# Performance work log

Hardware: AMD Instinct MI355X
Metric: run time of the kernel (lower is better)

The kernel has to match this reference:

```python
import jax, jax.numpy as jnp
import numpy as np
from jax.scipy.special import logsumexp

NEG = -10000.0  # LARGENUMBER in the torch code (finite, avoids NaN grads)


def _inside_Z(rules, sequence_lengths):
    """Log-semiring CKY inside algorithm (the `coolio` path of the torch module).

    rules: (B, S, S) span mention scores.
    chart[b,i,j] = inside score of span [i, j] where each span multiplies in
    (1 + exp(rule)) i.e. adds softplus(rule) (mention OR non-mention), and
    binarization sums over split points:
        chart[i,i] = softplus(rules[i,i])
        chart[i,j] = softplus(rules[i,j]) + logsumexp_{k=i..j-1}(chart[i,k] + chart[k+1,j])
    This matches: initial inside_s = logsumexp([rules, 0]) on the upper triangle,
    then width-wise logbmminside + diagonal add of log1p(exp(rules)).
    """
    B, S, _ = rules.shape
    idx = jnp.arange(S)
    sp = jax.nn.softplus(rules)  # log1p(exp(rules)), stable
    chart0 = jnp.full((B, S, S), NEG, dtype=rules.dtype)
    chart0 = chart0.at[:, idx, idx].set(jnp.diagonal(sp, axis1=1, axis2=2))

    def step(chart, w):
        # end position j = i + w (clipped; clipped rows are masked out below)
        j = jnp.clip(idx + w, 0, S - 1)                      # (S,)
        right = jnp.take(chart, j, axis=2)                   # right[b,k,i] = chart[b,k,i+w]
        right = jnp.concatenate([right[:, 1:, :], jnp.full_like(right[:, :1, :], NEG)], axis=1)  # chart[b,k+1,i+w]
        # scores[b,i,k] = chart[b,i,k] + chart[b,k+1,i+w]
        scores = chart + jnp.swapaxes(right, 1, 2)
        # valid split points: i <= k < i + w
        kmask = (idx[None, :] >= idx[:, None]) & (idx[None, :] < idx[:, None] + w)
        scores = jnp.where(kmask[None], scores, NEG)
        new_diag = logsumexp(scores, axis=2) + sp[:, idx, j]  # (B, S)
        valid = (idx + w) < S
        old = chart[:, idx, j]
        chart = chart.at[:, idx, j].set(jnp.where(valid[None, :], new_diag, old))
        return chart, None

    chart, _ = jax.lax.scan(step, chart0, jnp.arange(1, S))
    Z = chart[jnp.arange(B), 0, sequence_lengths - 1]  # log partition per sentence
    return Z


def setup_inputs():
    key = jax.random.key(0)
    k1, k2 = jax.random.split(key)
    B, S = 16, 192
    span = jax.random.normal(k1, (B, S, S, 1), dtype=jnp.float32)
    lens = jax.random.randint(k2, (B,), S // 2, S + 1).astype(jnp.int32)
    lens = lens.at[0].set(S)  # max length equals padded dim, as the torch module assumes
    return {"span_mention_score_matrix": span, "sequence_lengths": lens}


def reference(span_mention_score_matrix, sequence_lengths):
    # score_dim == 1 -> squeeze; marginal = d(sum Z)/d(rules), as in torch.autograd.grad
    rules = span_mention_score_matrix[..., 0]

    def f(r):
        Z = _inside_Z(r, sequence_lengths)
        return Z.sum(), Z

    (_, Z), marginal = jax.value_and_grad(f, has_aux=True)(rules)
    return Z, marginal
```

## Files before the change

kernel.cpp:

```cpp
#include <hip/hip_runtime.h>


#define SS 192
#define BB 16
#define TT 16
#define NTL 12
#define NEGF (-1e30f)

__device__ __forceinline__ float softplusf(float x) {
  return fmaxf(x, 0.f) + log1pf(__expf(-fabsf(x)));
}
__device__ __forceinline__ void lse_merge(float& m, float& s, float m2, float s2) {
  float nm = fmaxf(m, m2);
  s = s * __expf(m - nm) + s2 * __expf(m2 - nm);
  m = nm;
}
template <int CTRL>
__device__ __forceinline__ float dppf(float x) {
  return __int_as_float(__builtin_amdgcn_update_dpp(
      0, __float_as_int(x), CTRL, 0xF, 0xF, true));
}

__global__ __launch_bounds__(256) void init_od(float* __restrict__ odG,
                                               float* __restrict__ odTG) {
  const int n4 = BB * SS * SS / 4;
  float4 nf = make_float4(NEGF, NEGF, NEGF, NEGF);
  float4* a = reinterpret_cast<float4*>(odG);
  float4* c = reinterpret_cast<float4*>(odTG);
  for (int i = blockIdx.x * 256 + threadIdx.x; i < n4; i += gridDim.x * 256) {
    a[i] = nf; c[i] = nf;
  }
}

__global__ __launch_bounds__(256) void inside_diag(const float* __restrict__ rules,
                                                   float* __restrict__ chG_,
                                                   float* __restrict__ chTG_,
                                                   int d) {
  const int ntiles = NTL - d;
  const int b = blockIdx.x / ntiles;
  const int I = blockIdx.x % ntiles;
  const int J = I + d;
  const int tid = threadIdx.x;
  const int ci = tid >> 4, cj = tid & 15;
  const int gi = TT * I + ci, gj = TT * J + cj;
  const float* __restrict__ R = rules + (size_t)b * SS * SS;
  float* __restrict__ chG  = chG_  + (size_t)b * SS * SS;
  float* __restrict__ chTG = chTG_ + (size_t)b * SS * SS;

  __shared__ float A[TT][TT + 1], Bt[TT][TT + 1], T[TT][TT + 1];
  __shared__ float P[TT][TT + 1], SP[TT][TT + 1];
  __shared__ float brow[TT];

  const float spv_own = softplusf(R[gi * SS + gj]);
  SP[ci][cj] = spv_own;
  T[ci][cj] = (d == 0 && ci == cj) ? spv_own : NEGF;
  if (d >= 1) {
    A[ci][cj]  = chG[(TT * I + ci) * SS + TT * I + cj];
    Bt[ci][cj] = chG[(TT * J + ci) * SS + TT * J + cj];
  }
  if (d >= 2 && tid < TT) brow[tid] = chG[(TT * (I + 1)) * SS + TT * J + tid];

  {
    float m = NEGF, s = 0.f;
    const float* chRow  = chG  + gi * SS;
    const float* chTRow = chTG + gj * SS;
    const int k0 = TT * (I + 1), k1 = TT * J;
    if (k0 < k1) {
      float4 blo = *reinterpret_cast<const float4*>(chTRow + k0);
      for (int k = k0; k < k1; k += 4) {
        float4 a4  = *reinterpret_cast<const float4*>(chRow + k);
        float4 bhi = *reinterpret_cast<const float4*>(chTRow + k + 4);
        float v0 = a4.x + blo.y, v1 = a4.y + blo.z;
        float v2 = a4.z + blo.w, v3 = a4.w + bhi.x;
        float bm = fmaxf(fmaxf(v0, v1), fmaxf(v2, v3));
        float bs = __expf(v0 - bm) + __expf(v1 - bm) +
                   __expf(v2 - bm) + __expf(v3 - bm);
        lse_merge(m, s, bm, bs);
        blo = bhi;
      }
    }
    P[ci][cj] = (m < -1e29f) ? NEGF : m + __logf(s);
  }
  __syncthreads();

  if (tid < 64) {
    const int cidx = tid >> 2, g = tid & 3;
    const int s0 = (d == 0) ? TT : 0;
    for (int st = s0; st <= 30; ++st) {
      int ilmin = 15 - st; if (ilmin < 0) ilmin = 0;
      int ilmax = 30 - st; if (ilmax > 15) ilmax = 15;
      bool act = (cidx <= ilmax - ilmin);
      int tci = ilmin + (act ? cidx : 0);
      int tcj = tci + st - 15;
      int c1 = (d == 0) ? (st - 15) : (TT - tci);
      int c2 = (d == 0) ? 0 : tcj;
      int nt = c1 + c2;
      float m  = (g == 0) ? P[tci][tcj] : NEGF;
      float sa = (g == 0) ? 1.f : 0.f;
      float tv[8];
      #pragma unroll
      for (int u = 0; u < 8; ++u) {
        int t = g + 4 * u;
        bool ok = act && (t < nt);
        int tc = ok ? t : 0;
        float va, vb;
        if (tc < c1) {
          int kk = tci + tc;
          va = (d == 0) ? T[tci][kk] : A[tci][kk];
          int r2 = kk + 1;
          if (r2 <= 15) vb = T[r2][tcj];
          else          vb = (d == 1) ? Bt[0][tcj] : brow[tcj];
        } else {
          int tp = tc - c1;
          va = T[tci][tp];
          vb = Bt[tp + 1][tcj];
        }
        tv[u] = ok ? (va + vb) : NEGF;
      }
      float m0 = fmaxf(tv[0], tv[1]), m1 = fmaxf(tv[2], tv[3]);
      float m2 = fmaxf(tv[4], tv[5]), m3 = fmaxf(tv[6], tv[7]);
      float bm = fmaxf(fmaxf(m0, m1), fmaxf(m2, m3));
      float bs = (__expf(tv[0] - bm) + __expf(tv[1] - bm)) +
                 (__expf(tv[2] - bm) + __expf(tv[3] - bm)) +
                 (__expf(tv[4] - bm) + __expf(tv[5] - bm)) +
                 (__expf(tv[6] - bm) + __expf(tv[7] - bm));
      lse_merge(m, sa, bm, bs);
      lse_merge(m, sa, dppf<0xB1>(m), dppf<0xB1>(sa));
      lse_merge(m, sa, dppf<0x4E>(m), dppf<0x4E>(sa));
      if (act && g == 0)
        T[tci][tcj] = SP[tci][tcj] + m + __logf(sa);
      __builtin_amdgcn_wave_barrier();
    }
  }
  __syncthreads();
  chG [gi * SS + gj] = T[ci][cj];
  chTG[gj * SS + gi] = T[ci][cj];
}

__global__ __launch_bounds__(256) void outside_diag(const float* __restrict__ rules,
                                                    const int* __restrict__ lens,
                                                    const float* __restrict__ chG_,
                                                    const float* __restrict__ chTG_,
                                                    float* __restrict__ odG_,
                                                    float* __restrict__ odTG_,
                                                    int d) {
  const int ntiles = NTL - d;
  const int b = blockIdx.x / ntiles;
  const int I = blockIdx.x % ntiles;
  const int J = I + d;
  const int L = lens[b];
  if (TT * J >= L) return;
  const int tid = threadIdx.x;
  const int ci = tid >> 4, cj = tid & 15;
  const int gi = TT * I + ci, gj = TT * J + cj;
  const float* __restrict__ R = rules + (size_t)b * SS * SS;
  const float* __restrict__ chG  = chG_  + (size_t)b * SS * SS;
  const float* __restrict__ chTG = chTG_ + (size_t)b * SS * SS;
  float* __restrict__ odG  = odG_  + (size_t)b * SS * SS;
  float* __restrict__ odTG = odTG_ + (size_t)b * SS * SS;

  __shared__ float A[TT][TT + 1], Bt[TT][TT + 1], T[TT][TT + 1];
  __shared__ float P[TT][TT + 1], SP[TT][TT + 1];

  const float spv_own = softplusf(R[gi * SS + gj]);
  SP[ci][cj] = spv_own;
  A[ci][cj]  = chG[(TT * I + ci) * SS + TT * I + cj];
  Bt[ci][cj] = chG[(TT * J + ci) * SS + TT * J + cj];
  const bool isroot = (gi == 0) && (gj == L - 1);
  T[ci][cj] = isroot ? spv_own : NEGF;

  {
    float m = NEGF, s = 0.f;
    const float* odRow    = odG + gi * SS;
    const float* chRowJ1  = chG + (gj + 1) * SS;
    const int p0 = TT * (J + 1);
    for (int p = p0; p < SS; p += 4) {
      float4 o4 = *reinterpret_cast<const float4*>(odRow + p);
      float4 c4 = *reinterpret_cast<const float4*>(chRowJ1 + p);
      float v0 = o4.x + c4.x, v1 = o4.y + c4.y;
      float v2 = o4.z + c4.z, v3 = o4.w + c4.w;
      float bm = fmaxf(fmaxf(v0, v1), fmaxf(v2, v3));
      float bs = __expf(v0 - bm) + __expf(v1 - bm) +
                 __expf(v2 - bm) + __expf(v3 - bm);
      lse_merge(m, s, bm, bs);
    }
    const float* odTRow   = odTG + gj * SS;
    const float* chTRowI1 = chTG + (gi - 1) * SS;
    const int aEnd = TT * I;
    for (int a = 0; a < aEnd; a += 4) {
      float4 o4 = *reinterpret_cast<const float4*>(odTRow + a);
      float4 c4 = *reinterpret_cast<const float4*>(chTRowI1 + a);
      float v0 = o4.x + c4.x, v1 = o4.y + c4.y;
      float v2 = o4.z + c4.z, v3 = o4.w + c4.w;
      float bm = fmaxf(fmaxf(v0, v1), fmaxf(v2, v3));
      float bs = __expf(v0 - bm) + __expf(v1 - bm) +
                 __expf(v2 - bm) + __expf(v3 - bm);
      lse_merge(m, s, bm, bs);
    }
    P[ci][cj] = (m < -1e29f) ? NEGF : m + __logf(s);
  }
  __syncthreads();

  if (tid < 64) {
    const int cidx = tid >> 2, g = tid & 3;
    const int sEnd = (d == 0) ? 15 : 0;
    for (int st = 30; st >= sEnd; --st) {
      int ilmin = 15 - st; if (ilmin < 0) ilmin = 0;
      int ilmax = 30 - st; if (ilmax > 15) ilmax = 15;
      bool act = (cidx <= ilmax - ilmin);
      int tci = ilmin + (act ? cidx : 0);
      int tcj = tci + st - 15;
      int tgi = TT * I + tci, tgj = TT * J + tcj;
      bool rooted = (tgi == 0 && tgj == L - 1);
      bool dowrite = act && (tgj < L) && !rooted;
      int c1 = 15 - tcj, c2 = tci;
      int nt = c1 + c2;
      float m  = (g == 0) ? P[tci][tcj] : NEGF;
      float sa = (g == 0) ? 1.f : 0.f;
      int cim1 = (tci > 0) ? tci - 1 : 0;
      float tv[8];
      #pragma unroll
      for (int u = 0; u < 8; ++u) {
        int t = g + 4 * u;
        bool ok = act && (t < nt);
        int tc = ok ? t : 0;
        float va, vb;
        if (tc < c1) {
          int pl = tcj + 1 + tc;
          va = T[tci][pl];
          vb = Bt[tcj + 1][pl];
        } else {
          int al = tc - c1;
          va = T[al][tcj];
          vb = A[al][cim1];
        }
        tv[u] = ok ? (va + vb) : NEGF;
      }
      float m0 = fmaxf(tv[0], tv[1]), m1 = fmaxf(tv[2], tv[3]);
      float m2 = fmaxf(tv[4], tv[5]), m3 = fmaxf(tv[6], tv[7]);
      float bm = fmaxf(fmaxf(m0, m1), fmaxf(m2, m3));
      float bs = (__expf(tv[0] - bm) + __expf(tv[1] - bm)) +
                 (__expf(tv[2] - bm) + __expf(tv[3] - bm)) +
                 (__expf(tv[4] - bm) + __expf(tv[5] - bm)) +
                 (__expf(tv[6] - bm) + __expf(tv[7] - bm));
      lse_merge(m, sa, bm, bs);
      lse_merge(m, sa, dppf<0xB1>(m), dppf<0xB1>(sa));
      lse_merge(m, sa, dppf<0x4E>(m), dppf<0x4E>(sa));
      if (dowrite && g == 0)
        T[tci][tcj] = SP[tci][tcj] + m + __logf(sa);
      __builtin_amdgcn_wave_barrier();
    }
  }
  __syncthreads();
  odG [gi * SS + gj] = T[ci][cj];
  odTG[gj * SS + gi] = T[ci][cj];
}

__global__ __launch_bounds__(256) void cky_marg(const float* __restrict__ rules,
                                                const int* __restrict__ lens,
                                                const float* __restrict__ chG_,
                                                const float* __restrict__ odG_,
                                                float* __restrict__ outZ,
                                                float* __restrict__ marg) {
  const int total = BB * SS * SS;
  for (int idx = blockIdx.x * 256 + threadIdx.x; idx < total; idx += gridDim.x * 256) {
    int b = idx / (SS * SS);
    int rem = idx - b * SS * SS;
    int i = rem / SS, j = rem - i * SS;
    int L = lens[b];
    if (rem == 0) outZ[b] = chG_[(size_t)b * SS * SS + (L - 1)];
    float val = 0.f;
    if (i <= j && j < L) {
      float r = rules[idx];
      float sp = softplusf(r);
      float Z = chG_[(size_t)b * SS * SS + (L - 1)];
      float o = odG_[idx] - sp;
      float c = chG_[idx];
      float sig = 1.f / (1.f + __expf(-r));
      val = sig * __expf(o + c - Z);
    }
    marg[idx] = val;
  }
}

extern "C" void kernel_launch(void* const* d_in, const int* in_sizes, int n_in,
                              void* d_out, int out_size, void* d_ws, size_t ws_size,
                              hipStream_t stream) {
  const float* rules = (const float*)d_in[0];
  const int* lens = (const int*)d_in[1];
  float* outZ = (float*)d_out;
  float* marg = (float*)d_out + BB;

  float* chG_  = (float*)d_ws;
  float* chTG_ = chG_  + (size_t)BB * SS * SS;
  float* odG_  = chTG_ + (size_t)BB * SS * SS;
  float* odTG_ = odG_  + (size_t)BB * SS * SS;

  init_od<<<256, 256, 0, stream>>>(odG_, odTG_);
  for (int d = 0; d < NTL; ++d)
    inside_diag<<<BB * (NTL - d), 256, 0, stream>>>(rules, chG_, chTG_, d);
  for (int d = NTL - 1; d >= 0; --d)
    outside_diag<<<BB * (NTL - d), 256, 0, stream>>>(rules, lens, chG_, chTG_,
                                                     odG_, odTG_, d);
  cky_marg<<<(BB * SS * SS + 255) / 256, 256, 0, stream>>>(rules, lens, chG_,
                                                           odG_, outZ, marg);
}
```

Measured before the change: 931.5 us.

## Fuse all CKY diagonal launches into one cooperative kernel with grid syncs

Replaces the 26 separate kernel launches (init, 12 inside diagonals, 12 outside diagonals, marginal) with a single cooperative kernel of BB*NTL blocks that loops over diagonals and uses grid-wide syncs between them. This is meant to remove per-launch overhead and inter-kernel gaps, which dominate for these small, latency-bound diagonal steps. In exchange, the final marginal pass and the init now run on only 192 blocks, and grid.sync carries its own cost.

```diff
diff --git a/kernel.cpp b/kernel.cpp
--- a/kernel.cpp
+++ b/kernel.cpp
@@ -1,10 +1,14 @@
 #include <hip/hip_runtime.h>
-
+#include <hip/hip_cooperative_groups.h>
+
+
+namespace cg = cooperative_groups;
 
 #define SS 192
 #define BB 16
 #define TT 16
 #define NTL 12
+#define NBLK (BB * NTL)
 #define NEGF (-1e30f)
 
 __device__ __forceinline__ float softplusf(float x) {
@@ -21,265 +25,263 @@
       0, __float_as_int(x), CTRL, 0xF, 0xF, true));
 }
 
-__global__ __launch_bounds__(256) void init_od(float* __restrict__ odG,
-                                               float* __restrict__ odTG) {
-  const int n4 = BB * SS * SS / 4;
-  float4 nf = make_float4(NEGF, NEGF, NEGF, NEGF);
-  float4* a = reinterpret_cast<float4*>(odG);
-  float4* c = reinterpret_cast<float4*>(odTG);
-  for (int i = blockIdx.x * 256 + threadIdx.x; i < n4; i += gridDim.x * 256) {
-    a[i] = nf; c[i] = nf;
-  }
-}
-
-__global__ __launch_bounds__(256) void inside_diag(const float* __restrict__ rules,
-                                                   float* __restrict__ chG_,
-                                                   float* __restrict__ chTG_,
-                                                   int d) {
-  const int ntiles = NTL - d;
-  const int b = blockIdx.x / ntiles;
-  const int I = blockIdx.x % ntiles;
-  const int J = I + d;
+__global__ __launch_bounds__(256) void cky_all(const float* __restrict__ rules,
+                                               const int* __restrict__ lens,
+                                               float* __restrict__ chGb,
+                                               float* __restrict__ chTGb,
+                                               float* __restrict__ odGb,
+                                               float* __restrict__ odTGb,
+                                               float* __restrict__ outZ,
+                                               float* __restrict__ marg) {
+  cg::grid_group grid = cg::this_grid();
+  const int bid = blockIdx.x;
   const int tid = threadIdx.x;
   const int ci = tid >> 4, cj = tid & 15;
-  const int gi = TT * I + ci, gj = TT * J + cj;
-  const float* __restrict__ R = rules + (size_t)b * SS * SS;
-  float* __restrict__ chG  = chG_  + (size_t)b * SS * SS;
-  float* __restrict__ chTG = chTG_ + (size_t)b * SS * SS;
 
   __shared__ float A[TT][TT + 1], Bt[TT][TT + 1], T[TT][TT + 1];
   __shared__ float P[TT][TT + 1], SP[TT][TT + 1];
   __shared__ float brow[TT];
 
-  const float spv_own = softplusf(R[gi * SS + gj]);
-  SP[ci][cj] = spv_own;
-  T[ci][cj] = (d == 0 && ci == cj) ? spv_own : NEGF;
-  if (d >= 1) {
-    A[ci][cj]  = chG[(TT * I + ci) * SS + TT * I + cj];
-    Bt[ci][cj] = chG[(TT * J + ci) * SS + TT * J + cj];
+  {
+    const int n4 = BB * SS * SS / 4;
+    float4 nf = make_float4(NEGF, NEGF, NEGF, NEGF);
+    float4* a = reinterpret_cast<float4*>(odGb);
+    float4* c = reinterpret_cast<float4*>(odTGb);
+    for (int i = bid * 256 + tid; i < n4; i += NBLK * 256) { a[i] = nf; c[i] = nf; }
   }
-  if (d >= 2 && tid < TT) brow[tid] = chG[(TT * (I + 1)) * SS + TT * J + tid];
+  grid.sync();
+
+  for (int d = 0; d < NTL; ++d) {
+    const int ntiles = NTL - d;
+    if (bid < BB * ntiles) {
+      const int b = bid / ntiles;
+      const int I = bid % ntiles;
+      const int J = I + d;
+      const int gi = TT * I + ci, gj = TT * J + cj;
+      const float* __restrict__ R = rules + (size_t)b * SS * SS;
+      float* __restrict__ chG  = chGb  + (size_t)b * SS * SS;
+      float* __restrict__ chTG = chTGb + (size_t)b * SS * SS;
+
+      const float spv_own = softplusf(R[gi * SS + gj]);
+      SP[ci][cj] = spv_own;
+      T[ci][cj] = (d == 0 && ci == cj) ? spv_own : NEGF;
+      if (d >= 1) {
+        A[ci][cj]  = chG[(TT * I + ci) * SS + TT * I + cj];
+        Bt[ci][cj] = chG[(TT * J + ci) * SS + TT * J + cj];
+      }
+      if (d >= 2 && tid < TT) brow[tid] = chG[(TT * (I + 1)) * SS + TT * J + tid];
+
+      {
+        float m = NEGF, s = 0.f;
+        const float* chRow  = chG  + gi * SS;
+        const float* chTRow = chTG + gj * SS;
+        const int k0 = TT * (I + 1), k1 = TT * J;
+        if (k0 < k1) {
+          float4 blo = *reinterpret_cast<const float4*>(chTRow + k0);
+          for (int k = k0; k < k1; k += 4) {
+            float4 a4  = *reinterpret_cast<const float4*>(chRow + k);
+            float4 bhi = *reinterpret_cast<const float4*>(chTRow + k + 4);
+            float v0 = a4.x + blo.y, v1 = a4.y + blo.z;
+            float v2 = a4.z + blo.w, v3 = a4.w + bhi.x;
+            float bm = fmaxf(fmaxf(v0, v1), fmaxf(v2, v3));
+            float bs = __expf(v0 - bm) + __expf(v1 - bm) +
+                       __expf(v2 - bm) + __expf(v3 - bm);
+            lse_merge(m, s, bm, bs);
+            blo = bhi;
+          }
+        }
+        P[ci][cj] = (m < -1e29f) ? NEGF : m + __logf(s);
+      }
+      __syncthreads();
+
+      if (tid < 64) {
+        const int cidx = tid >> 2, g = tid & 3;
+        const int s0 = (d == 0) ? TT : 0;
+        for (int st = s0; st <= 30; ++st) {
+          int ilmin = 15 - st; if (ilmin < 0) ilmin = 0;
+          int ilmax = 30 - st; if (ilmax > 15) ilmax = 15;
+          bool act = (cidx <= ilmax - ilmin);
+          int tci = ilmin + (act ? cidx : 0);
+          int tcj = tci + st - 15;
+          int c1 = (d == 0) ? (st - 15) : (TT - tci);
+          int c2 = (d == 0) ? 0 : tcj;
+          int nt = c1 + c2;
+          float m  = (g == 0) ? P[tci][tcj] : NEGF;
+          float sa = (g == 0) ? 1.f : 0.f;
+          float tv[8];
+          #pragma unroll
+          for (int u = 0; u < 8; ++u) {
+            int t = g + 4 * u;
+            bool ok = act && (t < nt);
+            int tc = ok ? t : 0;
+            float va, vb;
+            if (tc < c1) {
+              int kk = tci + tc;
+              va = (d == 0) ? T[tci][kk] : A[tci][kk];
+              int r2 = kk + 1;
+              if (r2 <= 15) vb = T[r2][tcj];
+              else          vb = (d == 1) ? Bt[0][tcj] : brow[tcj];
+            } else {
+              int tp = tc - c1;
+              va = T[tci][tp];
+              vb = Bt[tp + 1][tcj];
+            }
+            tv[u] = ok ? (va + vb) : NEGF;
+          }
+          float m0 = fmaxf(tv[0], tv[1]), m1 = fmaxf(tv[2], tv[3]);
+          float m2 = fmaxf(tv[4], tv[5]), m3 = fmaxf(tv[6], tv[7]);
+          float bm = fmaxf(fmaxf(m0, m1), fmaxf(m2, m3));
+          float bs = (__expf(tv[0] - bm) + __expf(tv[1] - bm)) +
+                     (__expf(tv[2] - bm) + __expf(tv[3] - bm)) +
+                     (__expf(tv[4] - bm) + __expf(tv[5] - bm)) +
+                     (__expf(tv[6] - bm) + __expf(tv[7] - bm));
+          lse_merge(m, sa, bm, bs);
+          lse_merge(m, sa, dppf<0xB1>(m), dppf<0xB1>(sa));
+          lse_merge(m, sa, dppf<0x4E>(m), dppf<0x4E>(sa));
+          if (act && g == 0)
+            T[tci][tcj] = SP[tci][tcj] + m + __logf(sa);
+          __builtin_amdgcn_wave_barrier();
+        }
+      }
+      __syncthreads();
+      chG [gi * SS + gj] = T[ci][cj];
+      chTG[gj * SS + gi] = T[ci][cj];
+    }
+    grid.sync();
+  }
+
+  for (int d = NTL - 1; d >= 0; --d) {
+    const int ntiles = NTL - d;
+    if (bid < BB * ntiles) {
+      const int b = bid / ntiles;
+      const int I = bid % ntiles;
+      const int J = I + d;
+      const int L = lens[b];
+      if (TT * J < L) {
+        const int gi = TT * I + ci, gj = TT * J + cj;
+        const float* __restrict__ R = rules + (size_t)b * SS * SS;
+        const float* __restrict__ chG  = chGb  + (size_t)b * SS * SS;
+        const float* __restrict__ chTG = chTGb + (size_t)b * SS * SS;
+        float* __restrict__ odG  = odGb  + (size_t)b * SS * SS;
+        float* __restrict__ odTG = odTGb + (size_t)b * SS * SS;
+
+        const float spv_own = softplusf(R[gi * SS + gj]);
+        SP[ci][cj] = spv_own;
+        A[ci][cj]  = chG[(TT * I + ci) * SS + TT * I + cj];
+        Bt[ci][cj] = chG[(TT * J + ci) * SS + TT * J + cj];
+        const bool isroot = (gi == 0) && (gj == L - 1);
+        T[ci][cj] = isroot ? spv_own : NEGF;
+
+        {
+          float m = NEGF, s = 0.f;
+          const float* odRow   = odG + gi * SS;
+          const float* chRowJ1 = chG + (gj + 1) * SS;
+          const int p0 = TT * (J + 1);
+          for (int p = p0; p < SS; p += 4) {
+            float4 o4 = *reinterpret_cast<const float4*>(odRow + p);
+            float4 c4 = *reinterpret_cast<const float4*>(chRowJ1 + p);
+            float v0 = o4.x + c4.x, v1 = o4.y + c4.y;
+            float v2 = o4.z + c4.z, v3 = o4.w + c4.w;
+            float bm = fmaxf(fmaxf(v0, v1), fmaxf(v2, v3));
+            float bs = __expf(v0 - bm) + __expf(v1 - bm) +
+                       __expf(v2 - bm) + __expf(v3 - bm);
+            lse_merge(m, s, bm, bs);
+          }
+          const float* odTRow   = odTG + gj * SS;
+          const float* chTRowI1 = chTG + (gi - 1) * SS;
+          const int aEnd = TT * I;
+          for (int a = 0; a < aEnd; a += 4) {
+            float4 o4 = *reinterpret_cast<const float4*>(odTRow + a);
+            float4 c4 = *reinterpret_cast<const float4*>(chTRowI1 + a);
+            float v0 = o4.x + c4.x, v1 = o4.y + c4.y;
+            float v2 = o4.z + c4.z, v3 = o4.w + c4.w;
+            float bm = fmaxf(fmaxf(v0, v1), fmaxf(v2, v3));
+            float bs = __expf(v0 - bm) + __expf(v1 - bm) +
+                       __expf(v2 - bm) + __expf(v3 - bm);
+            lse_merge(m, s, bm, bs);
+          }
+          P[ci][cj] = (m < -1e29f) ? NEGF : m + __logf(s);
+        }
+        __syncthreads();
+
+        if (tid < 64) {
+          const int cidx = tid >> 2, g = tid & 3;
+          const int sEnd = (d == 0) ? 15 : 0;
+          for (int st = 30; st >= sEnd; --st) {
+            int ilmin = 15 - st; if (ilmin < 0) ilmin = 0;
+            int ilmax = 30 - st; if (ilmax > 15) ilmax = 15;
+            bool act = (cidx <= ilmax - ilmin);
+            int tci = ilmin + (act ? cidx : 0);
+            int tcj = tci + st - 15;
+            int tgi = TT * I + tci, tgj = TT * J + tcj;
+            bool rooted = (tgi == 0 && tgj == L - 1);
+            bool dowrite = act && (tgj < L) && !rooted;
+            int c1 = 15 - tcj, c2 = tci;
+            int nt = c1 + c2;
+            float m  = (g == 0) ? P[tci][tcj] : NEGF;
+            float sa = (g == 0) ? 1.f : 0.f;
+            int cim1 = (tci > 0) ? tci - 1 : 0;
+            float tv[8];
+            #pragma unroll
+            for (int u = 0; u < 8; ++u) {
+              int t = g + 4 * u;
+              bool ok = act && (t < nt);
+              int tc = ok ? t : 0;
+              float va, vb;
+              if (tc < c1) {
+                int pl = tcj + 1 + tc;
+                va = T[tci][pl];
+                vb = Bt[tcj + 1][pl];
+              } else {
+                int al = tc - c1;
+                va = T[al][tcj];
+                vb = A[al][cim1];
+              }
+              tv[u] = ok ? (va + vb) : NEGF;
+            }
+            float m0 = fmaxf(tv[0], tv[1]), m1 = fmaxf(tv[2], tv[3]);
+            float m2 = fmaxf(tv[4], tv[5]), m3 = fmaxf(tv[6], tv[7]);
+            float bm = fmaxf(fmaxf(m0, m1), fmaxf(m2, m3));
+            float bs = (__expf(tv[0] - bm) + __expf(tv[1] - bm)) +
+                       (__expf(tv[2] - bm) + __expf(tv[3] - bm)) +
+                       (__expf(tv[4] - bm) + __expf(tv[5] - bm)) +
+                       (__expf(tv[6] - bm) + __expf(tv[7] - bm));
+            lse_merge(m, sa, bm, bs);
+            lse_merge(m, sa, dppf<0xB1>(m), dppf<0xB1>(sa));
+            lse_merge(m, sa, dppf<0x4E>(m), dppf<0x4E>(sa));
+            if (dowrite && g == 0)
+              T[tci][tcj] = SP[tci][tcj] + m + __logf(sa);
+            __builtin_amdgcn_wave_barrier();
+          }
+        }
+        __syncthreads();
+        odG [gi * SS + gj] = T[ci][cj];
+        odTG[gj * SS + gi] = T[ci][cj];
+      }
+    }
+    grid.sync();
+  }
 
   {
-    float m = NEGF, s = 0.f;
-    const float* chRow  = chG  + gi * SS;
-    const float* chTRow = chTG + gj * SS;
-    const int k0 = TT * (I + 1), k1 = TT * J;
-    if (k0 < k1) {
-      float4 blo = *reinterpret_cast<const float4*>(chTRow + k0);
-      for (int k = k0; k < k1; k += 4) {
-        float4 a4  = *reinterpret_cast<const float4*>(chRow + k);
-        float4 bhi = *reinterpret_cast<const float4*>(chTRow + k + 4);
-        float v0 = a4.x + blo.y, v1 = a4.y + blo.z;
-        float v2 = a4.z + blo.w, v3 = a4.w + bhi.x;
-        float bm = fmaxf(fmaxf(v0, v1), fmaxf(v2, v3));
-        float bs = __expf(v0 - bm) + __expf(v1 - bm) +
-                   __expf(v2 - bm) + __expf(v3 - bm);
-        lse_merge(m, s, bm, bs);
-        blo = bhi;
-      }
+    const int total = BB * SS * SS;
+    for (int idx = bid * 256 + tid; idx < total; idx += NBLK * 256) {
+      int b = idx / (SS * SS);
+      int rem = idx - b * SS * SS;
+      int i = rem / SS, j = rem - i * SS;
+      int L = lens[b];
+      if (rem == 0) outZ[b] = chGb[(size_t)b * SS * SS + (L - 1)];
+      float val = 0.f;
+      if (i <= j && j < L) {
+        float r = rules[idx];
+        float sp = softplusf(r);
+        float Z = chGb[(size_t)b * SS * SS + (L - 1)];
+        float o = odGb[idx] - sp;
+        float c = chGb[idx];
+        float sig = 1.f / (1.f + __expf(-r));
+        val = sig * __expf(o + c - Z);
+      }
+      marg[idx] = val;
     }
-    P[ci][cj] = (m < -1e29f) ? NEGF : m + __logf(s);
-  }
-  __syncthreads();
-
-  if (tid < 64) {
-    const int cidx = tid >> 2, g = tid & 3;
-    const int s0 = (d == 0) ? TT : 0;
-    for (int st = s0; st <= 30; ++st) {
-      int ilmin = 15 - st; if (ilmin < 0) ilmin = 0;
-      int ilmax = 30 - st; if (ilmax > 15) ilmax = 15;
-      bool act = (cidx <= ilmax - ilmin);
-      int tci = ilmin + (act ? cidx : 0);
-      int tcj = tci + st - 15;
-      int c1 = (d == 0) ? (st - 15) : (TT - tci);
-      int c2 = (d == 0) ? 0 : tcj;
-      int nt = c1 + c2;
-      float m  = (g == 0) ? P[tci][tcj] : NEGF;
-      float sa = (g == 0) ? 1.f : 0.f;
-      float tv[8];
-      #pragma unroll
-      for (int u = 0; u < 8; ++u) {
-        int t = g + 4 * u;
-        bool ok = act && (t < nt);
-        int tc = ok ? t : 0;
-        float va, vb;
-        if (tc < c1) {
-          int kk = tci + tc;
-          va = (d == 0) ? T[tci][kk] : A[tci][kk];
-          int r2 = kk + 1;
-          if (r2 <= 15) vb = T[r2][tcj];
-          else          vb = (d == 1) ? Bt[0][tcj] : brow[tcj];
-        } else {
-          int tp = tc - c1;
-          va = T[tci][tp];
-          vb = Bt[tp + 1][tcj];
-        }
-        tv[u] = ok ? (va + vb) : NEGF;
-      }
-      float m0 = fmaxf(tv[0], tv[1]), m1 = fmaxf(tv[2], tv[3]);
-      float m2 = fmaxf(tv[4], tv[5]), m3 = fmaxf(tv[6], tv[7]);
-      float bm = fmaxf(fmaxf(m0, m1), fmaxf(m2, m3));
-      float bs = (__expf(tv[0] - bm) + __expf(tv[1] - bm)) +
-                 (__expf(tv[2] - bm) + __expf(tv[3] - bm)) +
-                 (__expf(tv[4] - bm) + __expf(tv[5] - bm)) +
-                 (__expf(tv[6] - bm) + __expf(tv[7] - bm));
-      lse_merge(m, sa, bm, bs);
-      lse_merge(m, sa, dppf<0xB1>(m), dppf<0xB1>(sa));
-      lse_merge(m, sa, dppf<0x4E>(m), dppf<0x4E>(sa));
-      if (act && g == 0)
-        T[tci][tcj] = SP[tci][tcj] + m + __logf(sa);
-      __builtin_amdgcn_wave_barrier();
-    }
-  }
-  __syncthreads();
-  chG [gi * SS + gj] = T[ci][cj];
-  chTG[gj * SS + gi] = T[ci][cj];
-}
-
-__global__ __launch_bounds__(256) void outside_diag(const float* __restrict__ rules,
-                                                    const int* __restrict__ lens,
-                                                    const float* __restrict__ chG_,
-                                                    const float* __restrict__ chTG_,
-                                                    float* __restrict__ odG_,
-                                                    float* __restrict__ odTG_,
-                                                    int d) {
-  const int ntiles = NTL - d;
-  const int b = blockIdx.x / ntiles;
-  const int I = blockIdx.x % ntiles;
-  const int J = I + d;
-  const int L = lens[b];
-  if (TT * J >= L) return;
-  const int tid = threadIdx.x;
-  const int ci = tid >> 4, cj = tid & 15;
-  const int gi = TT * I + ci, gj = TT * J + cj;
-  const float* __restrict__ R = rules + (size_t)b * SS * SS;
-  const float* __restrict__ chG  = chG_  + (size_t)b * SS * SS;
-  const float* __restrict__ chTG = chTG_ + (size_t)b * SS * SS;
-  float* __restrict__ odG  = odG_  + (size_t)b * SS * SS;
-  float* __restrict__ odTG = odTG_ + (size_t)b * SS * SS;
-
-  __shared__ float A[TT][TT + 1], Bt[TT][TT + 1], T[TT][TT + 1];
-  __shared__ float P[TT][TT + 1], SP[TT][TT + 1];
-
-  const float spv_own = softplusf(R[gi * SS + gj]);
-  SP[ci][cj] = spv_own;
-  A[ci][cj]  = chG[(TT * I + ci) * SS + TT * I + cj];
-  Bt[ci][cj] = chG[(TT * J + ci) * SS + TT * J + cj];
-  const bool isroot = (gi == 0) && (gj == L - 1);
-  T[ci][cj] = isroot ? spv_own : NEGF;
-
-  {
-    float m = NEGF, s = 0.f;
-    const float* odRow    = odG + gi * SS;
-    const float* chRowJ1  = chG + (gj + 1) * SS;
-    const int p0 = TT * (J + 1);
-    for (int p = p0; p < SS; p += 4) {
-      float4 o4 = *reinterpret_cast<const float4*>(odRow + p);
-      float4 c4 = *reinterpret_cast<const float4*>(chRowJ1 + p);
-      float v0 = o4.x + c4.x, v1 = o4.y + c4.y;
-      float v2 = o4.z + c4.z, v3 = o4.w + c4.w;
-      float bm = fmaxf(fmaxf(v0, v1), fmaxf(v2, v3));
-      float bs = __expf(v0 - bm) + __expf(v1 - bm) +
-                 __expf(v2 - bm) + __expf(v3 - bm);
-      lse_merge(m, s, bm, bs);
-    }
-    const float* odTRow   = odTG + gj * SS;
-    const float* chTRowI1 = chTG + (gi - 1) * SS;
-    const int aEnd = TT * I;
-    for (int a = 0; a < aEnd; a += 4) {
-      float4 o4 = *reinterpret_cast<const float4*>(odTRow + a);
-      float4 c4 = *reinterpret_cast<const float4*>(chTRowI1 + a);
-      float v0 = o4.x + c4.x, v1 = o4.y + c4.y;
-      float v2 = o4.z + c4.z, v3 = o4.w + c4.w;
-      float bm = fmaxf(fmaxf(v0, v1), fmaxf(v2, v3));
-      float bs = __expf(v0 - bm) + __expf(v1 - bm) +
-                 __expf(v2 - bm) + __expf(v3 - bm);
-      lse_merge(m, s, bm, bs);
-    }
-    P[ci][cj] = (m < -1e29f) ? NEGF : m + __logf(s);
-  }
-  __syncthreads();
-
-  if (tid < 64) {
-    const int cidx = tid >> 2, g = tid & 3;
-    const int sEnd = (d == 0) ? 15 : 0;
-    for (int st = 30; st >= sEnd; --st) {
-      int ilmin = 15 - st; if (ilmin < 0) ilmin = 0;
-      int ilmax = 30 - st; if (ilmax > 15) ilmax = 15;
-      bool act = (cidx <= ilmax - ilmin);
-      int tci = ilmin + (act ? cidx : 0);
-      int tcj = tci + st - 15;
-      int tgi = TT * I + tci, tgj = TT * J + tcj;
-      bool rooted = (tgi == 0 && tgj == L - 1);
-      bool dowrite = act && (tgj < L) && !rooted;
-      int c1 = 15 - tcj, c2 = tci;
-      int nt = c1 + c2;
-      float m  = (g == 0) ? P[tci][tcj] : NEGF;
-      float sa = (g == 0) ? 1.f : 0.f;
-      int cim1 = (tci > 0) ? tci - 1 : 0;
-      float tv[8];
-      #pragma unroll
-      for (int u = 0; u < 8; ++u) {
-        int t = g + 4 * u;
-        bool ok = act && (t < nt);
-        int tc = ok ? t : 0;
-        float va, vb;
-        if (tc < c1) {
-          int pl = tcj + 1 + tc;
-          va = T[tci][pl];
-          vb = Bt[tcj + 1][pl];
-        } else {
-          int al = tc - c1;
-          va = T[al][tcj];
-          vb = A[al][cim1];
-        }
-        tv[u] = ok ? (va + vb) : NEGF;
-      }
-      float m0 = fmaxf(tv[0], tv[1]), m1 = fmaxf(tv[2], tv[3]);
-      float m2 = fmaxf(tv[4], tv[5]), m3 = fmaxf(tv[6], tv[7]);
-      float bm = fmaxf(fmaxf(m0, m1), fmaxf(m2, m3));
-      float bs = (__expf(tv[0] - bm) + __expf(tv[1] - bm)) +
-                 (__expf(tv[2] - bm) + __expf(tv[3] - bm)) +
-                 (__expf(tv[4] - bm) + __expf(tv[5] - bm)) +
-                 (__expf(tv[6] - bm) + __expf(tv[7] - bm));
-      lse_merge(m, sa, bm, bs);
-      lse_merge(m, sa, dppf<0xB1>(m), dppf<0xB1>(sa));
-      lse_merge(m, sa, dppf<0x4E>(m), dppf<0x4E>(sa));
-      if (dowrite && g == 0)
-        T[tci][tcj] = SP[tci][tcj] + m + __logf(sa);
-      __builtin_amdgcn_wave_barrier();
-    }
-  }
-  __syncthreads();
-  odG [gi * SS + gj] = T[ci][cj];
-  odTG[gj * SS + gi] = T[ci][cj];
-}
-
-__global__ __launch_bounds__(256) void cky_marg(const float* __restrict__ rules,
-                                                const int* __restrict__ lens,
-                                                const float* __restrict__ chG_,
-                                                const float* __restrict__ odG_,
-                                                float* __restrict__ outZ,
-                                                float* __restrict__ marg) {
-  const int total = BB * SS * SS;
-  for (int idx = blockIdx.x * 256 + threadIdx.x; idx < total; idx += gridDim.x * 256) {
-    int b = idx / (SS * SS);
-    int rem = idx - b * SS * SS;
-    int i = rem / SS, j = rem - i * SS;
-    int L = lens[b];
-    if (rem == 0) outZ[b] = chG_[(size_t)b * SS * SS + (L - 1)];
-    float val = 0.f;
-    if (i <= j && j < L) {
-      float r = rules[idx];
-      float sp = softplusf(r);
-      float Z = chG_[(size_t)b * SS * SS + (L - 1)];
-      float o = odG_[idx] - sp;
-      float c = chG_[idx];
-      float sig = 1.f / (1.f + __expf(-r));
-      val = sig * __expf(o + c - Z);
-    }
-    marg[idx] = val;
   }
 }
 
@@ -296,12 +298,8 @@
   float* odG_  = chTG_ + (size_t)BB * SS * SS;
   float* odTG_ = odG_  + (size_t)BB * SS * SS;
 
-  init_od<<<256, 256, 0, stream>>>(odG_, odTG_);
-  for (int d = 0; d < NTL; ++d)
-    inside_diag<<<BB * (NTL - d), 256, 0, stream>>>(rules, chG_, chTG_, d);
-  for (int d = NTL - 1; d >= 0; --d)
-    outside_diag<<<BB * (NTL - d), 256, 0, stream>>>(rules, lens, chG_, chTG_,
-                                                     odG_, odTG_, d);
-  cky_marg<<<(BB * SS * SS + 255) / 256, 256, 0, stream>>>(rules, lens, chG_,
-                                                           odG_, outZ, marg);
-}
+  void* args[] = {(void*)&rules, (void*)&lens, (void*)&chG_, (void*)&chTG_,
+                  (void*)&odG_, (void*)&odTG_, (void*)&outZ, (void*)&marg};
+  hipLaunchCooperativeKernel(reinterpret_cast<void*>(cky_all),
+                             dim3(NBLK), dim3(256), args, 0, stream);
+}
```

After: 1.370 ms. 1.47x slower.
